# Optimization experiments

Hardware: AMD Instinct MI355X
Metric: run time of the kernel (lower is better)

The kernel has to match this reference:

```python
import jax, jax.numpy as jnp
import numpy as np
from jax import lax

B, P, C = 2, 512, 5                 # images, proposals/img, classes (incl. background)
IN_FEAT, REP = 12544, 1024          # 256*7*7 pooled features; TwoMLPHead width
H_IMG = W_IMG = 800.0
SCORE_THRESH, NMS_THRESH, DET_PER_IMG = 0.05, 0.5, 100
MIN_SIZE = 0.01
WX, WY, WW, WH = 10.0, 10.0, 5.0, 5.0
BBOX_CLIP = float(np.log(1000.0 / 16.0))
NEG = -1e9


def _make_boxes(key, n):
    k1, k2, k3, k4 = jax.random.split(key, 4)
    cx = jax.random.uniform(k1, (n,)) * W_IMG
    cy = jax.random.uniform(k2, (n,)) * H_IMG
    bw = jax.random.uniform(k3, (n,)) * 180.0 + 20.0
    bh = jax.random.uniform(k4, (n,)) * 180.0 + 20.0
    x1 = jnp.clip(cx - bw / 2, 0.0, W_IMG)
    y1 = jnp.clip(cy - bh / 2, 0.0, H_IMG)
    x2 = jnp.clip(cx + bw / 2, 0.0, W_IMG)
    y2 = jnp.clip(cy + bh / 2, 0.0, H_IMG)
    return jnp.stack([x1, y1, x2, y2], -1).astype(jnp.float32)


def setup_inputs() -> dict:
    ks = jax.random.split(jax.random.key(0), 12)
    box_features = jax.random.normal(ks[0], (B * P, IN_FEAT), jnp.float32)
    proposals = jnp.stack([_make_boxes(ks[1 + i], P) for i in range(B)])
    def w(k, shp):
        return (jax.random.normal(k, shp, jnp.float32) / np.sqrt(shp[0])).astype(jnp.float32)
    return {
        'box_features': box_features,
        'proposals': proposals,
        'W1': w(ks[3], (IN_FEAT, REP)), 'b1': jnp.zeros((REP,), jnp.float32),
        'W2': w(ks[4], (REP, REP)),     'b2': jnp.zeros((REP,), jnp.float32),
        'Wc': w(ks[5], (REP, C)),       'bc': jnp.zeros((C,), jnp.float32),
        'Wb': w(ks[6], (REP, 4 * C)),   'bb': jnp.zeros((4 * C,), jnp.float32),
    }


def box_iou(a, b):
    area_a = (a[:, 2] - a[:, 0]) * (a[:, 3] - a[:, 1])
    area_b = (b[:, 2] - b[:, 0]) * (b[:, 3] - b[:, 1])
    lt = jnp.maximum(a[:, None, :2], b[None, :, :2])
    rb = jnp.minimum(a[:, None, 2:], b[None, :, 2:])
    wh = jnp.clip(rb - lt, 0.0)
    inter = wh[..., 0] * wh[..., 1]
    return inter / (area_a[:, None] + area_b[None, :] - inter + 1e-9)


def decode(reg, props):
    # reg: [N, C, 4] raw deltas; props: [N, 4] xyxy  (torchvision BoxCoder.decode)
    w = props[:, 2] - props[:, 0]
    h = props[:, 3] - props[:, 1]
    cx = props[:, 0] + 0.5 * w
    cy = props[:, 1] + 0.5 * h
    dx, dy = reg[..., 0] / WX, reg[..., 1] / WY
    dw = jnp.minimum(reg[..., 2] / WW, BBOX_CLIP)
    dh = jnp.minimum(reg[..., 3] / WH, BBOX_CLIP)
    pcx = dx * w[:, None] + cx[:, None]
    pcy = dy * h[:, None] + cy[:, None]
    pw = jnp.exp(dw) * w[:, None]
    ph = jnp.exp(dh) * h[:, None]
    return jnp.stack([pcx - 0.5 * pw, pcy - 0.5 * ph, pcx + 0.5 * pw, pcy + 0.5 * ph], -1)


def postprocess_one(boxes, scores, labels):
    # boxes [M,4] (already clipped), scores [M], labels [M] int; fixed-size output.
    M = boxes.shape[0]
    ws = boxes[:, 2] - boxes[:, 0]
    hs = boxes[:, 3] - boxes[:, 1]
    valid = (scores > SCORE_THRESH) & (ws >= MIN_SIZE) & (hs >= MIN_SIZE)
    order = jnp.argsort(-scores)
    b, s, l, v = boxes[order], scores[order], labels[order], valid[order]
    # batched (per-class) NMS via class-offset trick
    off = l.astype(b.dtype)[:, None] * (max(H_IMG, W_IMG) + 1.0)
    iou = box_iou(b + off, b + off)
    idxs = jnp.arange(M)

    def body(i, keep):
        sup = (iou[i] > NMS_THRESH) & keep[i] & (idxs > i)
        return keep & ~sup

    keep = lax.fori_loop(0, M, body, v)
    sc = jnp.where(keep, s, NEG)
    top_s, top_i = lax.top_k(sc, DET_PER_IMG)
    ok = top_s > NEG / 2
    tb = jnp.where(ok[:, None], b[top_i], 0.0)
    tl = jnp.where(ok, l[top_i], 0)
    ts = jnp.where(ok, top_s, 0.0)
    return tb, ts, tl


def reference(box_features, proposals, W1, b1, W2, b2, Wc, bc, Wb, bb):
    # box_head: TwoMLPHead
    h = jax.nn.relu(box_features @ W1 + b1)
    h = jax.nn.relu(h @ W2 + b2)
    # box_predictor
    class_logits = h @ Wc + bc                       # [N, C]
    box_regression = (h @ Wb + bb).reshape(-1, C, 4)  # [N, C, 4]
    props = proposals.reshape(-1, 4)
    pred = decode(box_regression, props)             # [N, C, 4]
    # clip to image
    pred = jnp.stack([
        jnp.clip(pred[..., 0], 0.0, W_IMG), jnp.clip(pred[..., 1], 0.0, H_IMG),
        jnp.clip(pred[..., 2], 0.0, W_IMG), jnp.clip(pred[..., 3], 0.0, H_IMG)], -1)
    scores = jax.nn.softmax(class_logits, -1)        # [N, C]
    # drop background class, flatten proposal-major (matches torch reshape(-1,4))
    pb = pred[:, 1:, :].reshape(B, P * (C - 1), 4)
    sc = scores[:, 1:].reshape(B, P * (C - 1))
    labels = jnp.tile(jnp.arange(1, C, dtype=jnp.int32), P)  # [M]
    boxes_o, scores_o, labels_o = jax.vmap(postprocess_one, in_axes=(0, 0, None))(pb, sc, labels)
    return boxes_o, scores_o, labels_o
```

## Files before the change

### kernel.cpp

```cpp
#include <hip/hip_runtime.h>
#include <math.h>

#define NROWS 1024
#define K1    12544
#define REP   1024
#define NDET  2048
#define DETS  100
#define BBOX_CLIP_F 4.135166556742356f

typedef __attribute__((ext_vector_type(8))) short bf16x8;
typedef __attribute__((ext_vector_type(4))) float f32x4;

__device__ __forceinline__ unsigned short rne_bf16(float x) {
  unsigned u = __float_as_uint(x);
  u += 0x7fffu + ((u >> 16) & 1u);
  return (unsigned short)(u >> 16);
}
__device__ __forceinline__ float bf16f(unsigned short h) {
  return __uint_as_float(((unsigned)h) << 16);
}
__device__ __forceinline__ int swz(int r, int s) {
  return s ^ (r & 3) ^ ((r >> 2) & 3);
}
__device__ __forceinline__ void gload16(const void* g, void* lds) {
  __builtin_amdgcn_global_load_lds(
      (const __attribute__((address_space(1))) unsigned int*)g,
      (__attribute__((address_space(3))) unsigned int*)lds, 16, 0, 0);
}

__global__ __launch_bounds__(256) void pack_b(
    const float* __restrict__ W, unsigned short* __restrict__ Oh,
    unsigned short* __restrict__ Ol, int nKB) {
  __shared__ unsigned short th[32 * 36], tl[32 * 36];
  const int kb = blockIdx.x, n0 = blockIdx.y * 32;
  const int t = threadIdx.x;
  const int r = t >> 3, c4 = (t & 7) << 2;
  float4 v = *(const float4*)&W[(size_t)(kb * 32 + r) * REP + n0 + c4];
  float fv[4] = {v.x, v.y, v.z, v.w};
#pragma unroll
  for (int j = 0; j < 4; ++j) {
    unsigned short h = rne_bf16(fv[j]);
    th[(c4 + j) * 36 + r] = h;
    tl[(c4 + j) * 36 + r] = rne_bf16(fv[j] - bf16f(h));
  }
  __syncthreads();
  const int half = t >> 7;
  const int n_loc = (t & 127) >> 2, slot = t & 3;
  const unsigned short* src = (half ? tl : th) + n_loc * 36 + slot * 8;
  ushort4 u0 = *(const ushort4*)src;
  ushort4 u1 = *(const ushort4*)(src + 4);
  const int n = n0 + n_loc, rb = n >> 7, rr = n & 127;
  size_t chunk = ((size_t)(rb * nKB + kb)) * 512 + rr * 4 + swz(rr, slot);
  unsigned short* dst = (half ? Ol : Oh) + chunk * 8;
  *(ushort4*)dst = u0;
  *(ushort4*)(dst + 4) = u1;
}

__global__ __launch_bounds__(256) void pack_a(
    const float* __restrict__ A, unsigned short* __restrict__ Oh,
    unsigned short* __restrict__ Ol, int K, int nKB) {
  const int kb = blockIdx.x;
  const int r = blockIdx.y * 64 + (threadIdx.x >> 2);
  const int slot = threadIdx.x & 3;
  const float* p = A + (size_t)r * K + kb * 32 + slot * 8;
  float4 f0 = *(const float4*)p;
  float4 f1 = *(const float4*)(p + 4);
  float fv[8] = {f0.x, f0.y, f0.z, f0.w, f1.x, f1.y, f1.z, f1.w};
  ushort4 uh0, uh1, ul0, ul1;
  unsigned short hh[8], ll[8];
#pragma unroll
  for (int j = 0; j < 8; ++j) {
    hh[j] = rne_bf16(fv[j]);
    ll[j] = rne_bf16(fv[j] - bf16f(hh[j]));
  }
  uh0 = make_ushort4(hh[0], hh[1], hh[2], hh[3]);
  uh1 = make_ushort4(hh[4], hh[5], hh[6], hh[7]);
  ul0 = make_ushort4(ll[0], ll[1], ll[2], ll[3]);
  ul1 = make_ushort4(ll[4], ll[5], ll[6], ll[7]);
  const int rb = r >> 7, rr = r & 127;
  size_t chunk = ((size_t)(rb * nKB + kb)) * 512 + rr * 4 + swz(rr, slot);
  unsigned short* dh = Oh + chunk * 8;
  unsigned short* dl = Ol + chunk * 8;
  *(ushort4*)dh = uh0; *(ushort4*)(dh + 4) = uh1;
  *(ushort4*)dl = ul0; *(ushort4*)(dl + 4) = ul1;
}

__global__ __launch_bounds__(256) void gemm_pk2(
    const unsigned short* __restrict__ Ah, const unsigned short* __restrict__ Al,
    const unsigned short* __restrict__ Bh, const unsigned short* __restrict__ Bl,
    float* __restrict__ T, int nKB, int stepsPerZ) {
  __shared__ __align__(16) unsigned short lds[2][4][4096];
  const int tid = threadIdx.x;
  const int w = tid >> 6, l = tid & 63;
  const int rbA = blockIdx.x, rbB = blockIdx.y;
  const int tk0 = blockIdx.z * stepsPerZ;
  const int fr = l & 15, q = l >> 4;
  const int wr = (w >> 1) * 64, wc = (w & 1) * 64;
  const int qs = q ^ (fr & 3) ^ (fr >> 2);
  const int aoff = ((wr + fr) * 4 + qs) * 16;
  const int boff = ((wc + fr) * 4 + qs) * 16;

  auto stage = [&](int bf, int tk) {
    const unsigned short* ga_h = Ah + ((size_t)(rbA * nKB + tk)) * 4096;
    const unsigned short* ga_l = Al + ((size_t)(rbA * nKB + tk)) * 4096;
    const unsigned short* gb_h = Bh + ((size_t)(rbB * nKB + tk)) * 4096;
    const unsigned short* gb_l = Bl + ((size_t)(rbB * nKB + tk)) * 4096;
#pragma unroll
    for (int rseg = 0; rseg < 2; ++rseg) {
      const int seg = rseg * 4 + w;
      const size_t go = (size_t)(seg * 64 + l) * 8;
      gload16(ga_h + go, &lds[bf][0][seg * 512]);
      gload16(ga_l + go, &lds[bf][1][seg * 512]);
      gload16(gb_h + go, &lds[bf][2][seg * 512]);
      gload16(gb_l + go, &lds[bf][3][seg * 512]);
    }
  };

  f32x4 acc[4][4];
#pragma unroll
  for (int m = 0; m < 4; ++m)
#pragma unroll
    for (int n = 0; n < 4; ++n) acc[m][n] = (f32x4){0.f, 0.f, 0.f, 0.f};

  stage(0, tk0);
  __syncthreads();
  int cur = 0;
  for (int s = 0; s < stepsPerZ; ++s) {
    if (s + 1 < stepsPerZ) stage(cur ^ 1, tk0 + s + 1);
    const char* La  = (const char*)&lds[cur][0][0];
    const char* Ll  = (const char*)&lds[cur][1][0];
    const char* Lbh = (const char*)&lds[cur][2][0];
    const char* Lbl = (const char*)&lds[cur][3][0];
    bf16x8 ah[4], al[4], bh[4], bl[4];
#pragma unroll
    for (int m = 0; m < 4; ++m) {
      ah[m] = *(const bf16x8*)(La + aoff + m * 1024);
      al[m] = *(const bf16x8*)(Ll + aoff + m * 1024);
    }
#pragma unroll
    for (int n = 0; n < 4; ++n) {
      bh[n] = *(const bf16x8*)(Lbh + boff + n * 1024);
      bl[n] = *(const bf16x8*)(Lbl + boff + n * 1024);
    }
#pragma unroll
    for (int m = 0; m < 4; ++m)
#pragma unroll
      for (int n = 0; n < 4; ++n) {
        acc[m][n] = __builtin_amdgcn_mfma_f32_16x16x32_bf16(ah[m], bh[n], acc[m][n], 0, 0, 0);
        acc[m][n] = __builtin_amdgcn_mfma_f32_16x16x32_bf16(ah[m], bl[n], acc[m][n], 0, 0, 0);
        acc[m][n] = __builtin_amdgcn_mfma_f32_16x16x32_bf16(al[m], bh[n], acc[m][n], 0, 0, 0);
      }
    __syncthreads();
    cur ^= 1;
  }
  float* Tz = T + (size_t)blockIdx.z * (NROWS * REP);
#pragma unroll
  for (int m = 0; m < 4; ++m) {
    const int r0 = rbA * 128 + wr + m * 16 + ((l >> 4) << 2);
#pragma unroll
    for (int n = 0; n < 4; ++n) {
      const int c = rbB * 128 + wc + n * 16 + fr;
#pragma unroll
      for (int j = 0; j < 4; ++j) Tz[(size_t)(r0 + j) * REP + c] = acc[m][n][j];
    }
  }
}

__global__ __launch_bounds__(256) void combine8_relu_pack(
    const float* __restrict__ T, const float* __restrict__ bias,
    unsigned short* __restrict__ Oh, unsigned short* __restrict__ Ol) {
  const int e = (blockIdx.x * 256 + threadIdx.x) * 8;
  const int MN = NROWS * REP;
  float s[8];
  {
    float4 a0 = *(const float4*)&T[e];
    float4 a1 = *(const float4*)&T[e + 4];
    s[0] = a0.x; s[1] = a0.y; s[2] = a0.z; s[3] = a0.w;
    s[4] = a1.x; s[5] = a1.y; s[6] = a1.z; s[7] = a1.w;
  }
#pragma unroll
  for (int z = 1; z < 8; ++z) {
    float4 a0 = *(const float4*)&T[z * MN + e];
    float4 a1 = *(const float4*)&T[z * MN + e + 4];
    s[0] += a0.x; s[1] += a0.y; s[2] += a0.z; s[3] += a0.w;
    s[4] += a1.x; s[5] += a1.y; s[6] += a1.z; s[7] += a1.w;
  }
  const int c0 = e & 1023;
  float4 b0 = *(const float4*)&bias[c0];
  float4 b1 = *(const float4*)&bias[c0 + 4];
  s[0] = fmaxf(s[0] + b0.x, 0.f); s[1] = fmaxf(s[1] + b0.y, 0.f);
  s[2] = fmaxf(s[2] + b0.z, 0.f); s[3] = fmaxf(s[3] + b0.w, 0.f);
  s[4] = fmaxf(s[4] + b1.x, 0.f); s[5] = fmaxf(s[5] + b1.y, 0.f);
  s[6] = fmaxf(s[6] + b1.z, 0.f); s[7] = fmaxf(s[7] + b1.w, 0.f);
  unsigned short hh[8], ll[8];
#pragma unroll
  for (int j = 0; j < 8; ++j) {
    hh[j] = rne_bf16(s[j]);
    ll[j] = rne_bf16(s[j] - bf16f(hh[j]));
  }
  const int r = e >> 10;
  const int kb = c0 >> 5, slot = (c0 >> 3) & 3;
  const int rb = r >> 7, rr = r & 127;
  size_t chunk = ((size_t)(rb * 32 + kb)) * 512 + rr * 4 + swz(rr, slot);
  unsigned short* dh = Oh + chunk * 8;
  unsigned short* dl = Ol + chunk * 8;
  *(ushort4*)dh = make_ushort4(hh[0], hh[1], hh[2], hh[3]);
  *(ushort4*)(dh + 4) = make_ushort4(hh[4], hh[5], hh[6], hh[7]);
  *(ushort4*)dl = make_ushort4(ll[0], ll[1], ll[2], ll[3]);
  *(ushort4*)(dl + 4) = make_ushort4(ll[4], ll[5], ll[6], ll[7]);
}

__global__ __launch_bounds__(256) void combine8_relu(
    const float* __restrict__ T, const float* __restrict__ bias, float* __restrict__ H) {
  const int i = blockIdx.x * 256 + threadIdx.x;
  const int MN4 = NROWS * REP / 4;
  const float4* t = (const float4*)T;
  float4 s0 = t[i];
#pragma unroll
  for (int z = 1; z < 8; ++z) {
    float4 v = t[i + z * MN4];
    s0.x += v.x; s0.y += v.y; s0.z += v.z; s0.w += v.w;
  }
  float4 bs = ((const float4*)bias)[i & 255];
  float4 r;
  r.x = fmaxf(s0.x + bs.x, 0.f);
  r.y = fmaxf(s0.y + bs.y, 0.f);
  r.z = fmaxf(s0.z + bs.z, 0.f);
  r.w = fmaxf(s0.w + bs.w, 0.f);
  ((float4*)H)[i] = r;
}

__global__ __launch_bounds__(256) void gemm_pk(
    const float* __restrict__ A, const unsigned short* __restrict__ Bh,
    const unsigned short* __restrict__ Bl, float* __restrict__ T,
    int K, int nKB, int stepsPerZ) {
  __shared__ __align__(16) unsigned short lds[2][4][4096];
  const int tid = threadIdx.x;
  const int w = tid >> 6, l = tid & 63;
  const int bm = blockIdx.x * 128;
  const int bnb = blockIdx.y;
  const int tk0 = blockIdx.z * stepsPerZ;
  const int arow = tid >> 1, ahalf = tid & 1;
  const int fr = l & 15, q = l >> 4;
  const int wr = (w >> 1) * 64, wc = (w & 1) * 64;
  const int qs = q ^ (fr & 3) ^ (fr >> 2);
  const int aoff = ((wr + fr) * 4 + qs) * 16;
  const int boff = ((wc + fr) * 4 + qs) * 16;
  const float* aptr = A + (size_t)(bm + arow) * K + ahalf * 16;

  float4 av[4];
  auto loadA = [&](int tk) {
    const float* p = aptr + tk * 32;
#pragma unroll
    for (int j = 0; j < 4; ++j) av[j] = *(const float4*)(p + j * 4);
  };
  auto stageB = [&](int bf, int tk) {
    const unsigned short* gh = Bh + ((size_t)(bnb * nKB + tk)) * 4096;
    const unsigned short* gl_ = Bl + ((size_t)(bnb * nKB + tk)) * 4096;
#pragma unroll
    for (int rseg = 0; rseg < 2; ++rseg) {
      const int seg = rseg * 4 + w;
      gload16(gh + (size_t)(seg * 64 + l) * 8, &lds[bf][2][seg * 512]);
      gload16(gl_ + (size_t)(seg * 64 + l) * 8, &lds[bf][3][seg * 512]);
    }
  };
  auto writeA = [&](int bf) {
#pragma unroll
    for (int j = 0; j < 2; ++j) {
      const int s_ = ahalf * 2 + j;
      float fv[8] = {av[j * 2].x, av[j * 2].y, av[j * 2].z, av[j * 2].w,
                     av[j * 2 + 1].x, av[j * 2 + 1].y, av[j * 2 + 1].z, av[j * 2 + 1].w};
      unsigned hp[4], lp[4];
#pragma unroll
      for (int p2 = 0; p2 < 4; ++p2) {
        unsigned short h0 = rne_bf16(fv[2 * p2]), h1 = rne_bf16(fv[2 * p2 + 1]);
        float l0 = fv[2 * p2] - bf16f(h0), l1 = fv[2 * p2 + 1] - bf16f(h1);
        hp[p2] = (unsigned)h0 | ((unsigned)h1 << 16);
        lp[p2] = (unsigned)rne_bf16(l0) | ((unsigned)rne_bf16(l1) << 16);
      }
      const int chunk = arow * 4 + swz(arow, s_);
      *(uint4*)&lds[bf][0][chunk * 8] = make_uint4(hp[0], hp[1], hp[2], hp[3]);
      *(uint4*)&lds[bf][1][chunk * 8] = make_uint4(lp[0], lp[1], lp[2], lp[3]);
    }
  };

  f32x4 acc[4][4];
#pragma unroll
  for (int m = 0; m < 4; ++m)
#pragma unroll
    for (int n = 0; n < 4; ++n) acc[m][n] = (f32x4){0.f, 0.f, 0.f, 0.f};

  loadA(tk0);
  stageB(0, tk0);
  writeA(0);
  __syncthreads();
  int cur = 0;
  for (int s = 0; s < stepsPerZ; ++s) {
    const bool nx = (s + 1 < stepsPerZ);
    if (nx) { loadA(tk0 + s + 1); stageB(cur ^ 1, tk0 + s + 1); }
    const char* La = (const char*)&lds[cur][0][0];
    const char* Ll = (const char*)&lds[cur][1][0];
    const char* Lbh = (const char*)&lds[cur][2][0];
    const char* Lbl = (const char*)&lds[cur][3][0];
    bf16x8 ah[4], al[4], bh[4], bl[4];
#pragma unroll
    for (int m = 0; m < 4; ++m) {
      ah[m] = *(const bf16x8*)(La + aoff + m * 1024);
      al[m] = *(const bf16x8*)(Ll + aoff + m * 1024);
    }
#pragma unroll
    for (int n = 0; n < 4; ++n) {
      bh[n] = *(const bf16x8*)(Lbh + boff + n * 1024);
      bl[n] = *(const bf16x8*)(Lbl + boff + n * 1024);
    }
#pragma unroll
    for (int m = 0; m < 4; ++m)
#pragma unroll
      for (int n = 0; n < 4; ++n) {
        acc[m][n] = __builtin_amdgcn_mfma_f32_16x16x32_bf16(ah[m], bh[n], acc[m][n], 0, 0, 0);
        acc[m][n] = __builtin_amdgcn_mfma_f32_16x16x32_bf16(ah[m], bl[n], acc[m][n], 0, 0, 0);
        acc[m][n] = __builtin_amdgcn_mfma_f32_16x16x32_bf16(al[m], bh[n], acc[m][n], 0, 0, 0);
      }
    if (nx) writeA(cur ^ 1);
    __syncthreads();
    cur ^= 1;
  }
  float* Tz = T + (size_t)blockIdx.z * (NROWS * REP);
#pragma unroll
  for (int m = 0; m < 4; ++m) {
    const int r0 = bm + wr + m * 16 + ((l >> 4) << 2);
#pragma unroll
    for (int n = 0; n < 4; ++n) {
      const int c = bnb * 128 + wc + n * 16 + fr;
#pragma unroll
      for (int j = 0; j < 4; ++j) Tz[(size_t)(r0 + j) * REP + c] = acc[m][n][j];
    }
  }
}

__global__ __launch_bounds__(256) void gemm64(
    const float* __restrict__ A, const float* __restrict__ W,
    float* __restrict__ T, int K, int N, int kChunk) {
  __shared__ float As[32][68];
  __shared__ float Bs[32][64];
  const int tid = threadIdx.x;
  const int bm = blockIdx.x * 64, bn = blockIdx.y * 64;
  const int k0 = blockIdx.z * kChunk;
  const int tx = tid & 15, ty = tid >> 4;
  const int ar = tid >> 3;
  const int ac = (tid & 7) << 2;
  const int br = tid >> 4;
  const int bc = (tid & 15) << 2;
  float acc[4][4] = {{0.f,0.f,0.f,0.f},{0.f,0.f,0.f,0.f},{0.f,0.f,0.f,0.f},{0.f,0.f,0.f,0.f}};
  for (int kk = k0; kk < k0 + kChunk; kk += 32) {
    float4 a0 = *(const float4*)&A[(size_t)(bm + ar) * K + kk + ac];
    float4 a1 = *(const float4*)&A[(size_t)(bm + ar + 32) * K + kk + ac];
    float4 b0 = *(const float4*)&W[(size_t)(kk + br) * N + bn + bc];
    float4 b1 = *(const float4*)&W[(size_t)(kk + br + 16) * N + bn + bc];
    As[ac+0][ar] = a0.x; As[ac+1][ar] = a0.y; As[ac+2][ar] = a0.z; As[ac+3][ar] = a0.w;
    As[ac+0][ar+32] = a1.x; As[ac+1][ar+32] = a1.y; As[ac+2][ar+32] = a1.z; As[ac+3][ar+32] = a1.w;
    *(float4*)&Bs[br][bc]    = b0;
    *(float4*)&Bs[br+16][bc] = b1;
    __syncthreads();
#pragma unroll
    for (int k = 0; k < 32; ++k) {
      float4 av = *(const float4*)&As[k][ty << 2];
      float4 bv = *(const float4*)&Bs[k][tx << 2];
      float a_[4] = {av.x, av.y, av.z, av.w};
      float b_[4] = {bv.x, bv.y, bv.z, bv.w};
#pragma unroll
      for (int i = 0; i < 4; ++i)
#pragma unroll
        for (int j = 0; j < 4; ++j)
          acc[i][j] = fmaf(a_[i], b_[j], acc[i][j]);
    }
    __syncthreads();
  }
  float* Tz = T + (size_t)blockIdx.z * NROWS * REP;
#pragma unroll
  for (int i = 0; i < 4; ++i) {
    float4 v = make_float4(acc[i][0], acc[i][1], acc[i][2], acc[i][3]);
    *(float4*)&Tz[(size_t)(bm + (ty << 2) + i) * N + bn + (tx << 2)] = v;
  }
}

__global__ __launch_bounds__(256) void combine_relu(
    const float* __restrict__ T, const float* __restrict__ bias, float* __restrict__ H) {
  const int i = blockIdx.x * 256 + threadIdx.x;
  const int MN4 = NROWS * REP / 4;
  const float4* t = (const float4*)T;
  float4 a = t[i], b = t[i + MN4], c = t[i + 2 * MN4], d = t[i + 3 * MN4];
  float4 bs = ((const float4*)bias)[i & 255];
  float4 r;
  r.x = fmaxf(((a.x + b.x) + (c.x + d.x)) + bs.x, 0.f);
  r.y = fmaxf(((a.y + b.y) + (c.y + d.y)) + bs.y, 0.f);
  r.z = fmaxf(((a.z + b.z) + (c.z + d.z)) + bs.z, 0.f);
  r.w = fmaxf(((a.w + b.w) + (c.w + d.w)) + bs.w, 0.f);
  ((float4*)H)[i] = r;
}

__global__ __launch_bounds__(256) void heads_kernel(
    const float* __restrict__ H2, const float* __restrict__ Wc, const float* __restrict__ bcv,
    const float* __restrict__ Wb, const float* __restrict__ bbv,
    const float* __restrict__ props, float* __restrict__ pb, float* __restrict__ sc) {
  const int n = blockIdx.x;
  __shared__ float hrow[REP];
  __shared__ float part[25][8];
  __shared__ float outv[25];
  __shared__ float smax[5];
  const int tid = threadIdx.x;
  ((float4*)hrow)[tid] = ((const float4*)(H2 + (size_t)n * REP))[tid];
  __syncthreads();
  if (tid < 200) {
    const int o = tid >> 3, s = tid & 7;
    float a = 0.f;
    if (o < 5) {
      const float* w = Wc + o;
      for (int k = s * 128; k < s * 128 + 128; ++k) a = fmaf(hrow[k], w[(size_t)k * 5], a);
    } else {
      const float* w = Wb + (o - 5);
      for (int k = s * 128; k < s * 128 + 128; ++k) a = fmaf(hrow[k], w[(size_t)k * 20], a);
    }
    part[o][s] = a;
  }
  __syncthreads();
  if (tid < 25) {
    float a = ((part[tid][0] + part[tid][1]) + (part[tid][2] + part[tid][3]))
            + ((part[tid][4] + part[tid][5]) + (part[tid][6] + part[tid][7]));
    a += (tid < 5) ? bcv[tid] : bbv[tid - 5];
    outv[tid] = a;
  }
  __syncthreads();
  if (tid == 0) {
    float m = outv[0];
    for (int c = 1; c < 5; ++c) m = fmaxf(m, outv[c]);
    float e[5], ssum = 0.f;
    for (int c = 0; c < 5; ++c) { e[c] = expf(outv[c] - m); ssum += e[c]; }
    for (int c = 0; c < 5; ++c) smax[c] = e[c] / ssum;
  }
  __syncthreads();
  if (tid < 4) {
    const int c = tid + 1;
    const float* pr = props + (size_t)n * 4;
    const float x1 = pr[0], y1 = pr[1], x2 = pr[2], y2 = pr[3];
    const float w = x2 - x1, h = y2 - y1;
    const float cx = x1 + 0.5f * w, cy = y1 + 0.5f * h;
    const float r0 = outv[5 + c * 4 + 0], r1 = outv[5 + c * 4 + 1];
    const float r2 = outv[5 + c * 4 + 2], r3 = outv[5 + c * 4 + 3];
    const float dx = r0 / 10.0f, dy = r1 / 10.0f;
    const float dw = fminf(r2 / 5.0f, BBOX_CLIP_F);
    const float dh = fminf(r3 / 5.0f, BBOX_CLIP_F);
    const float pcx = dx * w + cx, pcy = dy * h + cy;
    const float pw = expf(dw) * w, ph = expf(dh) * h;
    float bx1 = pcx - 0.5f * pw, by1 = pcy - 0.5f * ph;
    float bx2 = pcx + 0.5f * pw, by2 = pcy + 0.5f * ph;
    bx1 = fminf(fmaxf(bx1, 0.f), 800.f);
    by1 = fminf(fmaxf(by1, 0.f), 800.f);
    bx2 = fminf(fmaxf(bx2, 0.f), 800.f);
    by2 = fminf(fmaxf(by2, 0.f), 800.f);
    const int img = n >> 9;
    const int pidx = ((n & 511) << 2) + (c - 1);
    float* o = pb + (size_t)(img * NDET + pidx) * 4;
    o[0] = bx1; o[1] = by1; o[2] = bx2; o[3] = by2;
    sc[img * NDET + pidx] = smax[c];
  }
}

__global__ __launch_bounds__(1024) void sort_kernel(
    const float* __restrict__ sc, unsigned* __restrict__ sidx) {
  const int b = blockIdx.x;
  __shared__ unsigned long long key[NDET];
  const int tid = threadIdx.x;
  for (int t = tid; t < NDET; t += 1024) {
    unsigned bits = __float_as_uint(sc[b * NDET + t]);
    key[t] = ((unsigned long long)bits << 32) | (unsigned)(~t);
  }
  __syncthreads();
  for (int k = 2; k <= NDET; k <<= 1) {
    for (int j = k >> 1; j > 0; j >>= 1) {
      for (int t = tid; t < NDET; t += 1024) {
        const int ixj = t ^ j;
        if (ixj > t) {
          const bool up = (t & k) == 0;
          unsigned long long a = key[t], bb_ = key[ixj];
          if ((a < bb_) == up) { key[t] = bb_; key[ixj] = a; }
        }
      }
      __syncthreads();
    }
  }
  for (int t = tid; t < NDET; t += 1024)
    sidx[b * NDET + t] = ~(unsigned)key[t];
}

__global__ __launch_bounds__(256) void prep_kernel(
    const unsigned* __restrict__ sidx, const float* __restrict__ pb, const float* __restrict__ sc,
    float* __restrict__ sbox, float* __restrict__ soff, float* __restrict__ sscore,
    float* __restrict__ sarea, float* __restrict__ slab, unsigned* __restrict__ vword) {
  const int b = blockIdx.y;
  const int i = blockIdx.x * 256 + threadIdx.x;
  const unsigned oi = sidx[b * NDET + i];
  const float* bx = pb + (size_t)(b * NDET + oi) * 4;
  const float x1 = bx[0], y1 = bx[1], x2 = bx[2], y2 = bx[3];
  const float s = sc[b * NDET + oi];
  const float lab = (float)((oi & 3) + 1);
  const bool valid = (s > 0.05f) && ((x2 - x1) >= 0.01f) && ((y2 - y1) >= 0.01f);
  const float off = lab * 801.0f;
  float* sb = sbox + (size_t)(b * NDET + i) * 4;
  sb[0] = x1; sb[1] = y1; sb[2] = x2; sb[3] = y2;
  float* so = soff + (size_t)(b * NDET + i) * 4;
  so[0] = x1 + off; so[1] = y1 + off; so[2] = x2 + off; so[3] = y2 + off;
  sscore[b * NDET + i] = s;
  sarea[b * NDET + i] = (x2 - x1) * (y2 - y1);
  slab[b * NDET + i] = lab;
  const unsigned long long bal = __ballot(valid);
  if ((i & 31) == 0) vword[b * 64 + (i >> 5)] = (unsigned)(bal >> (i & 32));
}

__global__ __launch_bounds__(256) void mask_kernel(
    const float* __restrict__ soff, const float* __restrict__ sarea,
    unsigned* __restrict__ mask) {
  const int b = blockIdx.y;
  __shared__ float box[NDET][4];
  __shared__ float area[NDET];
  const int tid = threadIdx.x;
  const float4* src = (const float4*)(soff + (size_t)b * NDET * 4);
  for (int t = tid; t < NDET; t += 256) ((float4*)box)[t] = src[t];
  const float4* asrc = (const float4*)(sarea + (size_t)b * NDET);
  for (int t = tid; t < NDET / 4; t += 256) ((float4*)area)[t] = asrc[t];
  __syncthreads();
  const int li = tid >> 6;
  const int w  = tid & 63;
  const int i  = blockIdx.x * 4 + li;
  const float ax1 = box[i][0], ay1 = box[i][1], ax2 = box[i][2], ay2 = box[i][3];
  const float aa = area[i];
  unsigned bits = 0;
#pragma unroll 4
  for (int jj = 0; jj < 32; ++jj) {
    const int j = jj * 64 + w;
    const float ix = fmaxf(fminf(ax2, box[j][2]) - fmaxf(ax1, box[j][0]), 0.f);
    const float iy = fmaxf(fminf(ay2, box[j][3]) - fmaxf(ay1, box[j][1]), 0.f);
    const float inter = ix * iy;
    const float iou = inter / (aa + area[j] - inter + 1e-9f);
    if (j > i && iou > 0.5f) bits |= (1u << jj);
  }
  mask[((size_t)b * NDET + i) * 64 + w] = bits;
}

__global__ __launch_bounds__(64) void scan_kernel(
    const unsigned* __restrict__ vword, const unsigned* __restrict__ mask,
    const float* __restrict__ sbox, const float* __restrict__ sscore,
    const float* __restrict__ slab, float* __restrict__ out) {
  const int b = blockIdx.x;
  const int lane = threadIdx.x;
  const unsigned valid = vword[b * 64 + lane];
  unsigned sup = 0;
  __shared__ unsigned short klist[DETS];
  int kcnt = 0;
  for (int i = 0; i < NDET; ++i) {
    const unsigned v = __shfl(valid, i >> 5);
    if (!((v >> (i & 31)) & 1)) continue;
    const unsigned s = __shfl(sup, i & 63);
    if ((s >> (i >> 6)) & 1) continue;
    if (lane == 0) klist[kcnt] = (unsigned short)i;
    kcnt++;
    sup |= mask[((size_t)b * NDET + i) * 64 + lane];
    if (kcnt == DETS) break;
  }
  __syncthreads();
  for (int s = lane; s < DETS; s += 64) {
    float b0 = 0.f, b1 = 0.f, b2 = 0.f, b3 = 0.f, sv = 0.f, lv = 0.f;
    if (s < kcnt) {
      const int i = klist[s];
      const float* bx = sbox + ((size_t)b * NDET + i) * 4;
      b0 = bx[0]; b1 = bx[1]; b2 = bx[2]; b3 = bx[3];
      sv = sscore[b * NDET + i];
      lv = slab[b * NDET + i];
    }
    float* ob = out + ((size_t)b * DETS + s) * 4;
    ob[0] = b0; ob[1] = b1; ob[2] = b2; ob[3] = b3;
    out[2 * DETS * 4 + b * DETS + s] = sv;
    out[2 * DETS * 4 + 2 * DETS + b * DETS + s] = lv;
  }
}

extern "C" void kernel_launch(void* const* d_in, const int* in_sizes, int n_in,
                              void* d_out, int out_size, void* d_ws, size_t ws_size,
                              hipStream_t stream) {
  const float* X     = (const float*)d_in[0];
  const float* props = (const float*)d_in[1];
  const float* W1    = (const float*)d_in[2];
  const float* b1    = (const float*)d_in[3];
  const float* W2    = (const float*)d_in[4];
  const float* b2    = (const float*)d_in[5];
  const float* Wc    = (const float*)d_in[6];
  const float* bc    = (const float*)d_in[7];
  const float* Wb    = (const float*)d_in[8];
  const float* bb    = (const float*)d_in[9];
  float* out = (float*)d_out;

  const size_t POST_B = 3000000;
  const size_t NEED_BIG =
      (size_t)9 * 1048576 * 4 +
      (size_t)4 * (size_t)K1 * 1024 * 2 +
      (size_t)4 * 1048576 * 2 + POST_B;
  const size_t NEED_MID =
      (size_t)10 * 1048576 * 4 +
      (size_t)2 * (size_t)K1 * 1024 * 2 +
      (size_t)2 * 1048576 * 2 + 2500000;

  float *T, *H1 = nullptr, *H2, *pb, *sc;
  unsigned short *W1h = nullptr, *W1l = nullptr, *W2h = nullptr, *W2l = nullptr;
  unsigned short *Ahp = nullptr, *Alp = nullptr, *H1h = nullptr, *H1l = nullptr;
  const int path = (ws_size >= NEED_BIG) ? 2 : (ws_size >= NEED_MID) ? 1 : 0;
  if (path == 2) {
    T   = (float*)d_ws;
    H2  = T + 8 * 1048576;
    W1h = (unsigned short*)(H2 + 1048576);
    W1l = W1h + (size_t)K1 * 1024;
    W2h = W1l + (size_t)K1 * 1024;
    W2l = W2h + 1048576;
    Ahp = W2l + 1048576;
    Alp = Ahp + (size_t)K1 * 1024;
    H1h = Alp + (size_t)K1 * 1024;
    H1l = H1h + 1048576;
    pb  = (float*)(H1l + 1048576);
  } else if (path == 1) {
    T   = (float*)d_ws;
    H1  = T + 8 * 1048576;
    H2  = H1 + 1048576;
    W1h = (unsigned short*)(H2 + 1048576);
    W1l = W1h + (size_t)K1 * 1024;
    W2h = W1l + (size_t)K1 * 1024;
    W2l = W2h + 1048576;
    pb  = (float*)(W2l + 1048576);
  } else {
    T  = (float*)d_ws;
    H1 = T + 4 * 1048576;
    H2 = H1 + 1048576;
    pb = H2 + 1048576;
  }
  sc = pb + 2 * NDET * 4;
  unsigned* sidx = (unsigned*)(sc + 2 * NDET);
  float* sbox   = (float*)(sidx + 2 * NDET);
  float* soff   = sbox + 2 * NDET * 4;
  float* sscore = soff + 2 * NDET * 4;
  float* sarea  = sscore + 2 * NDET;
  float* slab   = sarea + 2 * NDET;
  unsigned* vword = (unsigned*)(slab + 2 * NDET);
  unsigned* mask  = vword + 128;

  if (path == 2) {
    pack_b<<<dim3(K1 / 32, 32), 256, 0, stream>>>(W1, W1h, W1l, K1 / 32);
    pack_b<<<dim3(32, 32), 256, 0, stream>>>(W2, W2h, W2l, 32);
    pack_a<<<dim3(K1 / 32, 16), 256, 0, stream>>>(X, Ahp, Alp, K1, K1 / 32);
    gemm_pk2<<<dim3(8, 8, 8), 256, 0, stream>>>(Ahp, Alp, W1h, W1l, T, K1 / 32, 49);
    combine8_relu_pack<<<512, 256, 0, stream>>>(T, b1, H1h, H1l);
    gemm_pk2<<<dim3(8, 8, 8), 256, 0, stream>>>(H1h, H1l, W2h, W2l, T, 32, 4);
    combine8_relu<<<1024, 256, 0, stream>>>(T, b2, H2);
  } else if (path == 1) {
    pack_b<<<dim3(K1 / 32, 32), 256, 0, stream>>>(W1, W1h, W1l, K1 / 32);
    pack_b<<<dim3(32, 32), 256, 0, stream>>>(W2, W2h, W2l, 32);
    gemm_pk<<<dim3(8, 8, 8), 256, 0, stream>>>(X, W1h, W1l, T, K1, K1 / 32, 49);
    combine8_relu<<<1024, 256, 0, stream>>>(T, b1, H1);
    gemm_pk<<<dim3(8, 8, 8), 256, 0, stream>>>(H1, W2h, W2l, T, REP, 32, 4);
    combine8_relu<<<1024, 256, 0, stream>>>(T, b2, H2);
  } else {
    gemm64<<<dim3(16, 16, 4), 256, 0, stream>>>(X, W1, T, K1, REP, K1 / 4);
    combine_relu<<<1024, 256, 0, stream>>>(T, b1, H1);
    gemm64<<<dim3(16, 16, 4), 256, 0, stream>>>(H1, W2, T, REP, REP, REP / 4);
    combine_relu<<<1024, 256, 0, stream>>>(T, b2, H2);
  }
  heads_kernel<<<1024, 256, 0, stream>>>(H2, Wc, bc, Wb, bb, props, pb, sc);
  sort_kernel<<<2, 1024, 0, stream>>>(sc, sidx);
  prep_kernel<<<dim3(8, 2), 256, 0, stream>>>(sidx, pb, sc, sbox, soff, sscore, sarea, slab, vword);
  mask_kernel<<<dim3(512, 2), 256, 0, stream>>>(soff, sarea, mask);
  scan_kernel<<<2, 64, 0, stream>>>(vword, mask, sbox, sscore, slab, out);
}
```

Before: 253.5 us.

## Add wave-per-row heads kernel, remap GEMM tiles, and batch NMS mask rows

Adds a pack step that transposes the class and box head weights into a contiguous 25x1024 layout. A new heads kernel then computes one proposal row per wave, using float4 loads and a shuffle reduction instead of a per-block scalar loop. It also remaps the gemm_pk2 block indices so that neighbouring blocks share A and B tiles for better cache reuse. Finally, the mask kernel now handles 16 rows per block, cutting the grid size and the number of times each block reloads the box table into LDS. The cost is an extra pack launch and more workspace.

New measurement: 237.7 us. 1.07x faster.

```diff
diff --git a/kernel.cpp b/kernel.cpp
--- a/kernel.cpp
+++ b/kernel.cpp
@@ -66,23 +66,20 @@
   float4 f0 = *(const float4*)p;
   float4 f1 = *(const float4*)(p + 4);
   float fv[8] = {f0.x, f0.y, f0.z, f0.w, f1.x, f1.y, f1.z, f1.w};
-  ushort4 uh0, uh1, ul0, ul1;
   unsigned short hh[8], ll[8];
 #pragma unroll
   for (int j = 0; j < 8; ++j) {
     hh[j] = rne_bf16(fv[j]);
     ll[j] = rne_bf16(fv[j] - bf16f(hh[j]));
   }
-  uh0 = make_ushort4(hh[0], hh[1], hh[2], hh[3]);
-  uh1 = make_ushort4(hh[4], hh[5], hh[6], hh[7]);
-  ul0 = make_ushort4(ll[0], ll[1], ll[2], ll[3]);
-  ul1 = make_ushort4(ll[4], ll[5], ll[6], ll[7]);
   const int rb = r >> 7, rr = r & 127;
   size_t chunk = ((size_t)(rb * nKB + kb)) * 512 + rr * 4 + swz(rr, slot);
   unsigned short* dh = Oh + chunk * 8;
   unsigned short* dl = Ol + chunk * 8;
-  *(ushort4*)dh = uh0; *(ushort4*)(dh + 4) = uh1;
-  *(ushort4*)dl = ul0; *(ushort4*)(dl + 4) = ul1;
+  *(ushort4*)dh = make_ushort4(hh[0], hh[1], hh[2], hh[3]);
+  *(ushort4*)(dh + 4) = make_ushort4(hh[4], hh[5], hh[6], hh[7]);
+  *(ushort4*)dl = make_ushort4(ll[0], ll[1], ll[2], ll[3]);
+  *(ushort4*)(dl + 4) = make_ushort4(ll[4], ll[5], ll[6], ll[7]);
 }
 
 __global__ __launch_bounds__(256) void gemm_pk2(
@@ -92,7 +89,9 @@
   __shared__ __align__(16) unsigned short lds[2][4][4096];
   const int tid = threadIdx.x;
   const int w = tid >> 6, l = tid & 63;
-  const int rbA = blockIdx.x, rbB = blockIdx.y;
+  const int r_ = blockIdx.x, t_ = blockIdx.y;
+  const int rbA = (r_ & 3) * 2 + (t_ & 1);
+  const int rbB = (r_ >> 2) * 4 + (t_ >> 1);
   const int tk0 = blockIdx.z * stepsPerZ;
   const int fr = l & 15, q = l >> 4;
   const int wr = (w >> 1) * 64, wc = (w & 1) * 64;
@@ -399,6 +398,74 @@
   ((float4*)H)[i] = r;
 }
 
+__global__ __launch_bounds__(256) void pack_w25(
+    const float* __restrict__ Wc, const float* __restrict__ Wb, float* __restrict__ Wt) {
+  const int i = blockIdx.x * 256 + threadIdx.x;
+  if (i < 25 * 1024) {
+    const int o = i >> 10, k = i & 1023;
+    Wt[i] = (o < 5) ? Wc[(size_t)k * 5 + o] : Wb[(size_t)k * 20 + (o - 5)];
+  }
+}
+
+__global__ __launch_bounds__(256) void heads2(
+    const float* __restrict__ H2, const float* __restrict__ Wt,
+    const float* __restrict__ bcv, const float* __restrict__ bbv,
+    const float* __restrict__ props, float* __restrict__ pb, float* __restrict__ sc) {
+  const int wave = threadIdx.x >> 6, l = threadIdx.x & 63;
+  const int n = blockIdx.x * 4 + wave;
+  const float* h = H2 + (size_t)n * REP + l * 16;
+  float4 h0 = *(const float4*)h, h1 = *(const float4*)(h + 4);
+  float4 h2v = *(const float4*)(h + 8), h3 = *(const float4*)(h + 12);
+  float outv[25];
+#pragma unroll
+  for (int o = 0; o < 25; ++o) {
+    const float* wp = Wt + o * REP + l * 16;
+    float4 w0 = *(const float4*)wp, w1 = *(const float4*)(wp + 4);
+    float4 w2 = *(const float4*)(wp + 8), w3 = *(const float4*)(wp + 12);
+    float d = h0.x * w0.x;
+    d = fmaf(h0.y, w0.y, d); d = fmaf(h0.z, w0.z, d); d = fmaf(h0.w, w0.w, d);
+    d = fmaf(h1.x, w1.x, d); d = fmaf(h1.y, w1.y, d); d = fmaf(h1.z, w1.z, d); d = fmaf(h1.w, w1.w, d);
+    d = fmaf(h2v.x, w2.x, d); d = fmaf(h2v.y, w2.y, d); d = fmaf(h2v.z, w2.z, d); d = fmaf(h2v.w, w2.w, d);
+    d = fmaf(h3.x, w3.x, d); d = fmaf(h3.y, w3.y, d); d = fmaf(h3.z, w3.z, d); d = fmaf(h3.w, w3.w, d);
+#pragma unroll
+    for (int m = 1; m < 64; m <<= 1) d += __shfl_xor(d, m);
+    outv[o] = d + ((o < 5) ? bcv[o] : bbv[o - 5]);
+  }
+  const float mx = fmaxf(fmaxf(fmaxf(outv[0], outv[1]), fmaxf(outv[2], outv[3])), outv[4]);
+  const float e0 = expf(outv[0] - mx), e1 = expf(outv[1] - mx), e2 = expf(outv[2] - mx);
+  const float e3 = expf(outv[3] - mx), e4 = expf(outv[4] - mx);
+  const float inv = 1.0f / (e0 + e1 + e2 + e3 + e4);
+  const float s1 = e1 * inv, s2 = e2 * inv, s3 = e3 * inv, s4 = e4 * inv;
+  const float* pr = props + (size_t)n * 4;
+  const float x1 = pr[0], y1 = pr[1], x2 = pr[2], y2 = pr[3];
+  const float bw = x2 - x1, bh = y2 - y1;
+  const float cx = x1 + 0.5f * bw, cy = y1 + 0.5f * bh;
+  const int img = n >> 9, pbase = (n & 511) << 2;
+#pragma unroll
+  for (int c = 1; c <= 4; ++c) {
+    if (l == c - 1) {
+      const float r0 = outv[5 + c * 4 + 0], r1 = outv[5 + c * 4 + 1];
+      const float r2 = outv[5 + c * 4 + 2], r3 = outv[5 + c * 4 + 3];
+      const float dx = r0 / 10.0f, dy = r1 / 10.0f;
+      const float dw = fminf(r2 / 5.0f, BBOX_CLIP_F);
+      const float dh = fminf(r3 / 5.0f, BBOX_CLIP_F);
+      const float pcx = dx * bw + cx, pcy = dy * bh + cy;
+      const float pw = expf(dw) * bw, ph = expf(dh) * bh;
+      float bx1 = pcx - 0.5f * pw, by1 = pcy - 0.5f * ph;
+      float bx2 = pcx + 0.5f * pw, by2 = pcy + 0.5f * ph;
+      bx1 = fminf(fmaxf(bx1, 0.f), 800.f);
+      by1 = fminf(fmaxf(by1, 0.f), 800.f);
+      bx2 = fminf(fmaxf(bx2, 0.f), 800.f);
+      by2 = fminf(fmaxf(by2, 0.f), 800.f);
+      const int pidx = pbase + (c - 1);
+      float* o = pb + (size_t)(img * NDET + pidx) * 4;
+      o[0] = bx1; o[1] = by1; o[2] = bx2; o[3] = by2;
+      const float smc = (c == 1) ? s1 : (c == 2) ? s2 : (c == 3) ? s3 : s4;
+      sc[img * NDET + pidx] = smc;
+    }
+  }
+}
+
 __global__ __launch_bounds__(256) void heads_kernel(
     const float* __restrict__ H2, const float* __restrict__ Wc, const float* __restrict__ bcv,
     const float* __restrict__ Wb, const float* __restrict__ bbv,
@@ -531,20 +598,23 @@
   __syncthreads();
   const int li = tid >> 6;
   const int w  = tid & 63;
-  const int i  = blockIdx.x * 4 + li;
-  const float ax1 = box[i][0], ay1 = box[i][1], ax2 = box[i][2], ay2 = box[i][3];
-  const float aa = area[i];
-  unsigned bits = 0;
+#pragma unroll
+  for (int pass = 0; pass < 4; ++pass) {
+    const int i = blockIdx.x * 16 + pass * 4 + li;
+    const float ax1 = box[i][0], ay1 = box[i][1], ax2 = box[i][2], ay2 = box[i][3];
+    const float aa = area[i];
+    unsigned bits = 0;
 #pragma unroll 4
-  for (int jj = 0; jj < 32; ++jj) {
-    const int j = jj * 64 + w;
-    const float ix = fmaxf(fminf(ax2, box[j][2]) - fmaxf(ax1, box[j][0]), 0.f);
-    const float iy = fmaxf(fminf(ay2, box[j][3]) - fmaxf(ay1, box[j][1]), 0.f);
-    const float inter = ix * iy;
-    const float iou = inter / (aa + area[j] - inter + 1e-9f);
-    if (j > i && iou > 0.5f) bits |= (1u << jj);
-  }
-  mask[((size_t)b * NDET + i) * 64 + w] = bits;
+    for (int jj = 0; jj < 32; ++jj) {
+      const int j = jj * 64 + w;
+      const float ix = fmaxf(fminf(ax2, box[j][2]) - fmaxf(ax1, box[j][0]), 0.f);
+      const float iy = fmaxf(fminf(ay2, box[j][3]) - fmaxf(ay1, box[j][1]), 0.f);
+      const float inter = ix * iy;
+      const float iou = inter / (aa + area[j] - inter + 1e-9f);
+      if (j > i && iou > 0.5f) bits |= (1u << jj);
+    }
+    mask[((size_t)b * NDET + i) * 64 + w] = bits;
+  }
 }
 
 __global__ __launch_bounds__(64) void scan_kernel(
@@ -599,7 +669,7 @@
   const float* bb    = (const float*)d_in[9];
   float* out = (float*)d_out;
 
-  const size_t POST_B = 3000000;
+  const size_t POST_B = 3200000;
   const size_t NEED_BIG =
       (size_t)9 * 1048576 * 4 +
       (size_t)4 * (size_t)K1 * 1024 * 2 +
@@ -609,7 +679,7 @@
       (size_t)2 * (size_t)K1 * 1024 * 2 +
       (size_t)2 * 1048576 * 2 + 2500000;
 
-  float *T, *H1 = nullptr, *H2, *pb, *sc;
+  float *T, *H1 = nullptr, *H2, *pb, *sc, *Wt = nullptr;
   unsigned short *W1h = nullptr, *W1l = nullptr, *W2h = nullptr, *W2l = nullptr;
   unsigned short *Ahp = nullptr, *Alp = nullptr, *H1h = nullptr, *H1l = nullptr;
   const int path = (ws_size >= NEED_BIG) ? 2 : (ws_size >= NEED_MID) ? 1 : 0;
@@ -624,7 +694,8 @@
     Alp = Ahp + (size_t)K1 * 1024;
     H1h = Alp + (size_t)K1 * 1024;
     H1l = H1h + 1048576;
-    pb  = (float*)(H1l + 1048576);
+    Wt  = (float*)(H1l + 1048576);
+    pb  = Wt + 25 * 1024;
   } else if (path == 1) {
     T   = (float*)d_ws;
     H1  = T + 8 * 1048576;
@@ -654,10 +725,12 @@
     pack_b<<<dim3(K1 / 32, 32), 256, 0, stream>>>(W1, W1h, W1l, K1 / 32);
     pack_b<<<dim3(32, 32), 256, 0, stream>>>(W2, W2h, W2l, 32);
     pack_a<<<dim3(K1 / 32, 16), 256, 0, stream>>>(X, Ahp, Alp, K1, K1 / 32);
+    pack_w25<<<100, 256, 0, stream>>>(Wc, Wb, Wt);
     gemm_pk2<<<dim3(8, 8, 8), 256, 0, stream>>>(Ahp, Alp, W1h, W1l, T, K1 / 32, 49);
     combine8_relu_pack<<<512, 256, 0, stream>>>(T, b1, H1h, H1l);
     gemm_pk2<<<dim3(8, 8, 8), 256, 0, stream>>>(H1h, H1l, W2h, W2l, T, 32, 4);
     combine8_relu<<<1024, 256, 0, stream>>>(T, b2, H2);
+    heads2<<<256, 256, 0, stream>>>(H2, Wt, bc, bb, props, pb, sc);
   } else if (path == 1) {
     pack_b<<<dim3(K1 / 32, 32), 256, 0, stream>>>(W1, W1h, W1l, K1 / 32);
     pack_b<<<dim3(32, 32), 256, 0, stream>>>(W2, W2h, W2l, 32);
@@ -665,15 +738,16 @@
     combine8_relu<<<1024, 256, 0, stream>>>(T, b1, H1);
     gemm_pk<<<dim3(8, 8, 8), 256, 0, stream>>>(H1, W2h, W2l, T, REP, 32, 4);
     combine8_relu<<<1024, 256, 0, stream>>>(T, b2, H2);
+    heads_kernel<<<1024, 256, 0, stream>>>(H2, Wc, bc, Wb, bb, props, pb, sc);
   } else {
     gemm64<<<dim3(16, 16, 4), 256, 0, stream>>>(X, W1, T, K1, REP, K1 / 4);
     combine_relu<<<1024, 256, 0, stream>>>(T, b1, H1);
     gemm64<<<dim3(16, 16, 4), 256, 0, stream>>>(H1, W2, T, REP, REP, REP / 4);
     combine_relu<<<1024, 256, 0, stream>>>(T, b2, H2);
-  }
-  heads_kernel<<<1024, 256, 0, stream>>>(H2, Wc, bc, Wb, bb, props, pb, sc);
+    heads_kernel<<<1024, 256, 0, stream>>>(H2, Wc, bc, Wb, bb, props, pb, sc);
+  }
   sort_kernel<<<2, 1024, 0, stream>>>(sc, sidx);
   prep_kernel<<<dim3(8, 2), 256, 0, stream>>>(sidx, pb, sc, sbox, soff, sscore, sarea, slab, vword);
-  mask_kernel<<<dim3(512, 2), 256, 0, stream>>>(soff, sarea, mask);
+  mask_kernel<<<dim3(128, 2), 256, 0, stream>>>(soff, sarea, mask);
   scan_kernel<<<2, 64, 0, stream>>>(vword, mask, sbox, sscore, slab, out);
 }
```
